# Kernel tuning notes

Hardware: AMD Instinct MI355X
Metric: run time of the kernel (lower is better)

Reference implementation:

```python
import jax, jax.numpy as jnp
import numpy as np

N_NODES = 100000
IN_DIM = 256
HIDDEN = 256
EMBED = 128
N_EDGES = 500000


def setup_inputs() -> dict:
    key = jax.random.key(0)
    ks = jax.random.split(key, 16)
    inp = {
        "h": jax.random.normal(ks[0], (N_NODES, IN_DIM), dtype=jnp.float32),
        "pos_src": jax.random.randint(ks[1], (N_EDGES,), 0, N_NODES),
        "pos_dst": jax.random.randint(ks[2], (N_EDGES,), 0, N_NODES),
        "neg_src": jax.random.randint(ks[3], (N_EDGES,), 0, N_NODES),
        "neg_dst": jax.random.randint(ks[4], (N_EDGES,), 0, N_NODES),
        "node_embeddings": jax.random.normal(ks[5], (N_NODES, EMBED), dtype=jnp.float32) * 0.1,
        # nn.Linear params (torch convention: W [out, in], y = x @ W.T + b)
        "W_pos": jax.random.normal(ks[6], (HIDDEN, IN_DIM), dtype=jnp.float32) / np.sqrt(IN_DIM),
        "b_pos": jnp.zeros((HIDDEN,), dtype=jnp.float32),
        "W_neg": jax.random.normal(ks[7], (HIDDEN, IN_DIM), dtype=jnp.float32) / np.sqrt(IN_DIM),
        "b_neg": jnp.zeros((HIDDEN,), dtype=jnp.float32),
        "W_self": jax.random.normal(ks[8], (HIDDEN, IN_DIM), dtype=jnp.float32) / np.sqrt(IN_DIM),
        "b_self": jnp.zeros((HIDDEN,), dtype=jnp.float32),
        "w_pos_beta": jax.random.normal(ks[9], (EMBED,), dtype=jnp.float32) * 0.01,
        "W_pos_u": jax.random.normal(ks[10], (EMBED, EMBED), dtype=jnp.float32) * 0.01,
        "alpha_pos": jnp.array(1.0, dtype=jnp.float32),
        "w_neg_beta": jax.random.normal(ks[11], (EMBED,), dtype=jnp.float32) * 0.01,
        "W_neg_u": jax.random.normal(ks[12], (EMBED, EMBED), dtype=jnp.float32) * 0.01,
        "alpha_neg": jnp.array(1.0, dtype=jnp.float32),
    }
    return inp


def _finsler_weight(emb, src, dst, w_beta, W_u, alpha):
    # d_Fk(j,i) = ||x_i - x_j||_2 + beta_k(x_j) * <x_i - x_j, W_u x_j>
    x_j = emb[src]                                  # [E, D]
    x_i = emb[dst]                                  # [E, D]
    diff = x_i - x_j
    euclid = jnp.sqrt(jnp.sum(diff * diff, axis=-1))
    alpha_k = jnp.clip(alpha, 0.1, 10.0)
    beta_k = jnp.tanh(x_j @ w_beta)                 # [E]
    u_j = x_j @ W_u                                 # [E, D]
    asym = jnp.sum(diff * u_j, axis=-1)             # [E]
    d = euclid + beta_k * asym
    return jnp.exp(-alpha_k * jnp.maximum(d, 0.0))  # [E]


def _agg(h, src, dst, W, b, w, n):
    # gather -> linear -> weight -> scatter-add over dst
    msg = (h[src] @ W.T + b) * w[:, None]           # [E, H]
    return jax.ops.segment_sum(msg, dst, num_segments=n)


def reference(h, pos_src, pos_dst, neg_src, neg_dst, node_embeddings,
              W_pos, b_pos, W_neg, b_neg, W_self, b_self,
              w_pos_beta, W_pos_u, alpha_pos, w_neg_beta, W_neg_u, alpha_neg):
    n = h.shape[0]
    pos_w = _finsler_weight(node_embeddings, pos_src, pos_dst, w_pos_beta, W_pos_u, alpha_pos)
    neg_w = _finsler_weight(node_embeddings, neg_src, neg_dst, w_neg_beta, W_neg_u, alpha_neg)
    pos_msg = _agg(h, pos_src, pos_dst, W_pos, b_pos, pos_w, n)
    neg_msg = _agg(h, neg_src, neg_dst, W_neg, b_neg, neg_w, n)
    self_msg = h @ W_self.T + b_self
    return jax.nn.relu(pos_msg + neg_msg + self_msg)
```

## Files before the change

### kernel.cpp

```cpp
#include <hip/hip_runtime.h>
#include <hip/hip_bf16.h>
#include <stdint.h>

#define IN_DIM 256
#define HIDDEN 256
#define EMBED 128

__global__ __launch_bounds__(256) void gemm_bt(
    const float* __restrict__ A, const float* __restrict__ W,
    const float* __restrict__ bias, float* __restrict__ C,
    int M, int N, int K)
{
    __shared__ float Ast[16][68];
    __shared__ float Wst[16][68];
    const int tid = threadIdx.x;
    const int tx = tid & 15, ty = tid >> 4;
    const int m0 = blockIdx.x * 64, n0 = blockIdx.y * 64;

    const int lm = tid >> 2;
    const int lk = (tid & 3) << 2;

    float acc[4][4] = {};

    for (int k0 = 0; k0 < K; k0 += 16) {
        float4 av = make_float4(0.f, 0.f, 0.f, 0.f);
        const int am = m0 + lm;
        if (am < M) av = *(const float4*)&A[(size_t)am * K + k0 + lk];
        const float4 wv = *(const float4*)&W[(size_t)(n0 + lm) * K + k0 + lk];
        __syncthreads();
        Ast[lk + 0][lm] = av.x; Ast[lk + 1][lm] = av.y;
        Ast[lk + 2][lm] = av.z; Ast[lk + 3][lm] = av.w;
        Wst[lk + 0][lm] = wv.x; Wst[lk + 1][lm] = wv.y;
        Wst[lk + 2][lm] = wv.z; Wst[lk + 3][lm] = wv.w;
        __syncthreads();
#pragma unroll
        for (int k = 0; k < 16; ++k) {
            const float4 a = *(const float4*)&Ast[k][ty * 4];
            const float4 b = *(const float4*)&Wst[k][tx * 4];
            acc[0][0] += a.x * b.x; acc[0][1] += a.x * b.y; acc[0][2] += a.x * b.z; acc[0][3] += a.x * b.w;
            acc[1][0] += a.y * b.x; acc[1][1] += a.y * b.y; acc[1][2] += a.y * b.z; acc[1][3] += a.y * b.w;
            acc[2][0] += a.z * b.x; acc[2][1] += a.z * b.y; acc[2][2] += a.z * b.z; acc[2][3] += a.z * b.w;
            acc[3][0] += a.w * b.x; acc[3][1] += a.w * b.y; acc[3][2] += a.w * b.z; acc[3][3] += a.w * b.w;
        }
    }

    const float4 bv = *(const float4*)&bias[n0 + tx * 4];
#pragma unroll
    for (int i = 0; i < 4; ++i) {
        const int m = m0 + ty * 4 + i;
        if (m < M) {
            float4 o;
            o.x = acc[i][0] + bv.x; o.y = acc[i][1] + bv.y;
            o.z = acc[i][2] + bv.z; o.w = acc[i][3] + bv.w;
            *(float4*)&C[(size_t)m * N + n0 + tx * 4] = o;
        }
    }
}

__global__ __launch_bounds__(256) void gemm_nn(
    const float* __restrict__ A, const float* __restrict__ B,
    float* __restrict__ C, int M, int N, int K)
{
    __shared__ float Ast[16][68];
    __shared__ float Bs[16][68];
    const int tid = threadIdx.x;
    const int tx = tid & 15, ty = tid >> 4;
    const int m0 = blockIdx.x * 64, n0 = blockIdx.y * 64;

    const int lm = tid >> 2;
    const int lk = (tid & 3) << 2;
    const int bk = tid >> 4;
    const int bn = (tid & 15) << 2;

    float acc[4][4] = {};

    for (int k0 = 0; k0 < K; k0 += 16) {
        float4 av = make_float4(0.f, 0.f, 0.f, 0.f);
        const int am = m0 + lm;
        if (am < M) av = *(const float4*)&A[(size_t)am * K + k0 + lk];
        const float4 bvl = *(const float4*)&B[(size_t)(k0 + bk) * N + n0 + bn];
        __syncthreads();
        Ast[lk + 0][lm] = av.x; Ast[lk + 1][lm] = av.y;
        Ast[lk + 2][lm] = av.z; Ast[lk + 3][lm] = av.w;
        *(float4*)&Bs[bk][bn] = bvl;
        __syncthreads();
#pragma unroll
        for (int k = 0; k < 16; ++k) {
            const float4 a = *(const float4*)&Ast[k][ty * 4];
            const float4 b = *(const float4*)&Bs[k][tx * 4];
            acc[0][0] += a.x * b.x; acc[0][1] += a.x * b.y; acc[0][2] += a.x * b.z; acc[0][3] += a.x * b.w;
            acc[1][0] += a.y * b.x; acc[1][1] += a.y * b.y; acc[1][2] += a.y * b.z; acc[1][3] += a.y * b.w;
            acc[2][0] += a.z * b.x; acc[2][1] += a.z * b.y; acc[2][2] += a.z * b.z; acc[2][3] += a.z * b.w;
            acc[3][0] += a.w * b.x; acc[3][1] += a.w * b.y; acc[3][2] += a.w * b.z; acc[3][3] += a.w * b.w;
        }
    }

#pragma unroll
    for (int i = 0; i < 4; ++i) {
        const int m = m0 + ty * 4 + i;
        if (m < M) {
            float4 o;
            o.x = acc[i][0]; o.y = acc[i][1]; o.z = acc[i][2]; o.w = acc[i][3];
            *(float4*)&C[(size_t)m * N + n0 + tx * 4] = o;
        }
    }
}

__global__ __launch_bounds__(256) void edge_weight(
    const float* __restrict__ emb, const float* __restrict__ U,
    const float* __restrict__ w_beta, const float* __restrict__ alpha_p,
    const int* __restrict__ src, const int* __restrict__ dst,
    float* __restrict__ w_out, int E)
{
    const int wv = (int)((blockIdx.x * (size_t)blockDim.x + threadIdx.x) >> 6);
    const int lane = threadIdx.x & 63;
    if (wv >= E) return;
    const int s = src[wv], d = dst[wv];

    const float* xj = emb + (size_t)s * EMBED;
    const float* xi = emb + (size_t)d * EMBED;
    const float* uj = U + (size_t)s * EMBED;

    const float xj0 = xj[lane], xj1 = xj[lane + 64];
    const float xi0 = xi[lane], xi1 = xi[lane + 64];
    const float u0 = uj[lane],  u1 = uj[lane + 64];
    const float wb0 = w_beta[lane], wb1 = w_beta[lane + 64];

    const float d0 = xi0 - xj0, d1 = xi1 - xj1;
    float pe = d0 * d0 + d1 * d1;
    float pa = d0 * u0 + d1 * u1;
    float pb = xj0 * wb0 + xj1 * wb1;

#pragma unroll
    for (int off = 32; off > 0; off >>= 1) {
        pe += __shfl_xor(pe, off);
        pa += __shfl_xor(pa, off);
        pb += __shfl_xor(pb, off);
    }

    if (lane == 0) {
        const float alpha = fminf(fmaxf(alpha_p[0], 0.1f), 10.0f);
        const float beta = tanhf(pb);
        const float dist = sqrtf(pe) + beta * pa;
        w_out[wv] = expf(-alpha * fmaxf(dist, 0.0f));
    }
}

__global__ __launch_bounds__(256) void zero_int(int* __restrict__ p, int n)
{
    const int i = blockIdx.x * blockDim.x + threadIdx.x;
    if (i < n) p[i] = 0;
}

__global__ __launch_bounds__(256) void hist(
    const int* __restrict__ dst, int* __restrict__ counts, int E)
{
    const int e = blockIdx.x * blockDim.x + threadIdx.x;
    if (e < E) atomicAdd(&counts[dst[e]], 1);
}

__global__ __launch_bounds__(256) void scan1(
    const int* __restrict__ counts, int* __restrict__ offs,
    int* __restrict__ bsum, int n)
{
    __shared__ int wsum[4];
    const int t = threadIdx.x;
    const int gi = blockIdx.x * 1024 + t * 4;
    int v[4];
#pragma unroll
    for (int j = 0; j < 4; ++j) v[j] = (gi + j < n) ? counts[gi + j] : 0;
    const int local = v[0] + v[1] + v[2] + v[3];
    const int lane = t & 63;
    int x = local;
#pragma unroll
    for (int off = 1; off < 64; off <<= 1) {
        const int y = __shfl_up(x, off);
        if (lane >= off) x += y;
    }
    if (lane == 63) wsum[t >> 6] = x;
    __syncthreads();
    int woff = 0;
    const int wid = t >> 6;
    for (int w = 0; w < wid; ++w) woff += wsum[w];
    int run = woff + x - local;
#pragma unroll
    for (int j = 0; j < 4; ++j) {
        if (gi + j < n) offs[gi + j] = run;
        run += v[j];
    }
    if (t == 255) bsum[blockIdx.x] = woff + x;
}

__global__ __launch_bounds__(128) void scan2(int* __restrict__ bsum, int nb)
{
    __shared__ int tmp[128];
    const int t = threadIdx.x;
    tmp[t] = (t < nb) ? bsum[t] : 0;
    __syncthreads();
    if (t < nb) {
        int s = 0;
        for (int i = 0; i < t; ++i) s += tmp[i];
        bsum[t] = s;
    }
}

__global__ __launch_bounds__(256) void scan3(
    int* __restrict__ offs, int* __restrict__ cur,
    const int* __restrict__ bsum, int n, int E)
{
    const int gi = blockIdx.x * blockDim.x + threadIdx.x;
    if (gi < n) {
        const int v = offs[gi] + bsum[gi >> 10];
        offs[gi] = v;
        cur[gi] = v;
    }
    if (gi == 0) offs[n] = E;
}

__global__ __launch_bounds__(256) void place(
    const int* __restrict__ src, const int* __restrict__ dst,
    const float* __restrict__ w, int* __restrict__ cur,
    int* __restrict__ esrc, float* __restrict__ ew, int E)
{
    const int e = blockIdx.x * blockDim.x + threadIdx.x;
    if (e < E) {
        const int p = atomicAdd(&cur[dst[e]], 1);
        esrc[p] = src[e];
        ew[p] = w[e];
    }
}

template <bool RELU>
__global__ __launch_bounds__(256) void gather(
    const float* __restrict__ H, const int* __restrict__ offs,
    const int* __restrict__ esrc, const float* __restrict__ ew,
    float* __restrict__ out, int n)
{
    const int node = (int)((blockIdx.x * (size_t)blockDim.x + threadIdx.x) >> 6);
    const int lane = threadIdx.x & 63;
    if (node >= n) return;
    const int s0 = offs[node], s1 = offs[node + 1];

    float4 acc = make_float4(0.f, 0.f, 0.f, 0.f);
    for (int k = s0; k < s1; ++k) {
        const int s = esrc[k];
        const float wv = ew[k];
        const float4 v = *(const float4*)&H[(size_t)s * HIDDEN + lane * 4];
        acc.x += v.x * wv; acc.y += v.y * wv;
        acc.z += v.z * wv; acc.w += v.w * wv;
    }

    float* o = out + (size_t)node * HIDDEN + lane * 4;
    float4 c = *(const float4*)o;
    c.x += acc.x; c.y += acc.y; c.z += acc.z; c.w += acc.w;
    if (RELU) {
        c.x = fmaxf(c.x, 0.f); c.y = fmaxf(c.y, 0.f);
        c.z = fmaxf(c.z, 0.f); c.w = fmaxf(c.w, 0.f);
    }
    *(float4*)o = c;
}

extern "C" void kernel_launch(void* const* d_in, const int* in_sizes, int n_in,
                              void* d_out, int out_size, void* d_ws, size_t ws_size,
                              hipStream_t stream)
{
    const float* h        = (const float*)d_in[0];
    const int*   pos_src  = (const int*)d_in[1];
    const int*   pos_dst  = (const int*)d_in[2];
    const int*   neg_src  = (const int*)d_in[3];
    const int*   neg_dst  = (const int*)d_in[4];
    const float* emb      = (const float*)d_in[5];
    const float* W_pos    = (const float*)d_in[6];
    const float* b_pos    = (const float*)d_in[7];
    const float* W_neg    = (const float*)d_in[8];
    const float* b_neg    = (const float*)d_in[9];
    const float* W_self   = (const float*)d_in[10];
    const float* b_self   = (const float*)d_in[11];
    const float* w_pos_b  = (const float*)d_in[12];
    const float* W_pos_u  = (const float*)d_in[13];
    const float* alpha_p  = (const float*)d_in[14];
    const float* w_neg_b  = (const float*)d_in[15];
    const float* W_neg_u  = (const float*)d_in[16];
    const float* alpha_n  = (const float*)d_in[17];
    float* out = (float*)d_out;

    const int n_nodes = in_sizes[0] / IN_DIM;
    const int E       = in_sizes[1];

    float* ws     = (float*)d_ws;
    float* wpos   = ws;
    float* wneg   = wpos + E;
    int*   counts = (int*)(wneg + E);
    int*   offs   = counts + n_nodes;
    int*   cur    = offs + n_nodes + 1;
    int*   bsum   = cur + n_nodes;
    int*   esrc   = bsum + 128;
    float* ew     = (float*)(esrc + E);
    float* Hbuf   = (float*)(((uintptr_t)(ew + E) + 15) & ~(uintptr_t)15);
    float* Ubuf   = Hbuf;

    const dim3 blk(256);
    const dim3 gU((n_nodes + 63) / 64, EMBED / 64);
    const dim3 gH((n_nodes + 63) / 64, HIDDEN / 64);
    const dim3 gE((E + 3) / 4);
    const dim3 gEt((E + 255) / 256);
    const dim3 gN((n_nodes + 255) / 256);
    const dim3 gW((n_nodes + 3) / 4);
    const int  nb = (n_nodes + 1023) / 1024;

    gemm_nn<<<gU, blk, 0, stream>>>(emb, W_pos_u, Ubuf, n_nodes, EMBED, EMBED);
    edge_weight<<<gE, blk, 0, stream>>>(emb, Ubuf, w_pos_b, alpha_p,
                                        pos_src, pos_dst, wpos, E);
    gemm_nn<<<gU, blk, 0, stream>>>(emb, W_neg_u, Ubuf, n_nodes, EMBED, EMBED);
    edge_weight<<<gE, blk, 0, stream>>>(emb, Ubuf, w_neg_b, alpha_n,
                                        neg_src, neg_dst, wneg, E);

    gemm_bt<<<gH, blk, 0, stream>>>(h, W_self, b_self, out, n_nodes, HIDDEN, IN_DIM);

    zero_int<<<gN, blk, 0, stream>>>(counts, n_nodes);
    hist<<<gEt, blk, 0, stream>>>(pos_dst, counts, E);
    scan1<<<nb, blk, 0, stream>>>(counts, offs, bsum, n_nodes);
    scan2<<<1, 128, 0, stream>>>(bsum, nb);
    scan3<<<gN, blk, 0, stream>>>(offs, cur, bsum, n_nodes, E);
    place<<<gEt, blk, 0, stream>>>(pos_src, pos_dst, wpos, cur, esrc, ew, E);
    gemm_bt<<<gH, blk, 0, stream>>>(h, W_pos, b_pos, Hbuf, n_nodes, HIDDEN, IN_DIM);
    gather<false><<<gW, blk, 0, stream>>>(Hbuf, offs, esrc, ew, out, n_nodes);

    zero_int<<<gN, blk, 0, stream>>>(counts, n_nodes);
    hist<<<gEt, blk, 0, stream>>>(neg_dst, counts, E);
    scan1<<<nb, blk, 0, stream>>>(counts, offs, bsum, n_nodes);
    scan2<<<1, 128, 0, stream>>>(bsum, nb);
    scan3<<<gN, blk, 0, stream>>>(offs, cur, bsum, n_nodes, E);
    place<<<gEt, blk, 0, stream>>>(neg_src, neg_dst, wneg, cur, esrc, ew, E);
    gemm_bt<<<gH, blk, 0, stream>>>(h, W_neg, b_neg, Hbuf, n_nodes, HIDDEN, IN_DIM);
    gather<true><<<gW, blk, 0, stream>>>(Hbuf, offs, esrc, ew, out, n_nodes);
}
```

Baseline: 1.479 ms.

## Aggregate raw features before projection and fuse three GEMMs into one split-bf16 MFMA kernel

Uses linearity to gather and weight raw h rows per destination first, instead of projecting every node and then gathering. All three linear layers (pos, neg, self) then run as one concatenated-K GEMM, with the bias scaled by the per-node weight sums and ReLU applied in the epilogue. The GEMM moves from scalar FP32 FMA to bf16 MFMA using a hi/lo split with three products to keep near-FP32 accuracy, and the weights are pre-split in small kernels on each call. This removes two full HIDDEN-wide intermediate buffers and the read-modify-write passes over out, but adds two aggregated-feature buffers and B operands loaded straight from global memory without LDS reuse.

```diff
diff --git a/kernel.cpp b/kernel.cpp
--- a/kernel.cpp
+++ b/kernel.cpp
@@ -6,53 +6,103 @@
 #define HIDDEN 256
 #define EMBED 128
 
-__global__ __launch_bounds__(256) void gemm_bt(
-    const float* __restrict__ A, const float* __restrict__ W,
-    const float* __restrict__ bias, float* __restrict__ C,
-    int M, int N, int K)
-{
-    __shared__ float Ast[16][68];
-    __shared__ float Wst[16][68];
-    const int tid = threadIdx.x;
-    const int tx = tid & 15, ty = tid >> 4;
-    const int m0 = blockIdx.x * 64, n0 = blockIdx.y * 64;
-
-    const int lm = tid >> 2;
-    const int lk = (tid & 3) << 2;
-
-    float acc[4][4] = {};
-
-    for (int k0 = 0; k0 < K; k0 += 16) {
-        float4 av = make_float4(0.f, 0.f, 0.f, 0.f);
-        const int am = m0 + lm;
-        if (am < M) av = *(const float4*)&A[(size_t)am * K + k0 + lk];
-        const float4 wv = *(const float4*)&W[(size_t)(n0 + lm) * K + k0 + lk];
-        __syncthreads();
-        Ast[lk + 0][lm] = av.x; Ast[lk + 1][lm] = av.y;
-        Ast[lk + 2][lm] = av.z; Ast[lk + 3][lm] = av.w;
-        Wst[lk + 0][lm] = wv.x; Wst[lk + 1][lm] = wv.y;
-        Wst[lk + 2][lm] = wv.z; Wst[lk + 3][lm] = wv.w;
-        __syncthreads();
-#pragma unroll
-        for (int k = 0; k < 16; ++k) {
-            const float4 a = *(const float4*)&Ast[k][ty * 4];
-            const float4 b = *(const float4*)&Wst[k][tx * 4];
-            acc[0][0] += a.x * b.x; acc[0][1] += a.x * b.y; acc[0][2] += a.x * b.z; acc[0][3] += a.x * b.w;
-            acc[1][0] += a.y * b.x; acc[1][1] += a.y * b.y; acc[1][2] += a.y * b.z; acc[1][3] += a.y * b.w;
-            acc[2][0] += a.z * b.x; acc[2][1] += a.z * b.y; acc[2][2] += a.z * b.z; acc[2][3] += a.z * b.w;
-            acc[3][0] += a.w * b.x; acc[3][1] += a.w * b.y; acc[3][2] += a.w * b.z; acc[3][3] += a.w * b.w;
+using bf16x8 = __attribute__((ext_vector_type(8))) short;
+using f32x4  = __attribute__((ext_vector_type(4))) float;
+
+__device__ inline void split_bf16(float x, unsigned short& hb, unsigned short& lb)
+{
+    unsigned int u = __float_as_uint(x);
+    unsigned int r = u + 0x7fffu + ((u >> 16) & 1u);
+    hb = (unsigned short)(r >> 16);
+    float fh = __uint_as_float((unsigned int)hb << 16);
+    float xl = x - fh;
+    unsigned int ul = __float_as_uint(xl);
+    unsigned int rl = ul + 0x7fffu + ((ul >> 16) & 1u);
+    lb = (unsigned short)(rl >> 16);
+}
+
+__global__ __launch_bounds__(256) void conv_w(
+    const float* __restrict__ src, unsigned short* __restrict__ hi,
+    unsigned short* __restrict__ lo, int n)
+{
+    const int i = blockIdx.x * 256 + threadIdx.x;
+    if (i < n) {
+        unsigned short hb, lb;
+        split_bf16(src[i], hb, lb);
+        hi[i] = hb; lo[i] = lb;
+    }
+}
+
+__global__ __launch_bounds__(256) void mega_gemm(
+    const float* __restrict__ aggP, const float* __restrict__ aggN,
+    const float* __restrict__ h,
+    const unsigned short* __restrict__ Whi, const unsigned short* __restrict__ Wlo,
+    const float* __restrict__ b_pos, const float* __restrict__ b_neg,
+    const float* __restrict__ b_self,
+    const float* __restrict__ sw_pos, const float* __restrict__ sw_neg,
+    float* __restrict__ out, int M)
+{
+    const int tid  = threadIdx.x;
+    const int lane = tid & 63;
+    const int wid  = tid >> 6;
+    const int lr   = lane & 15;
+    const int lg   = lane >> 4;
+    const int m0   = blockIdx.x * 64;
+
+    const int rowA = min(m0 + wid * 16 + lr, M - 1);
+    const float* As[3] = {aggP, aggN, h};
+
+    f32x4 acc[16];
+#pragma unroll
+    for (int i = 0; i < 16; ++i) acc[i] = (f32x4){0.f, 0.f, 0.f, 0.f};
+
+#pragma unroll
+    for (int seg = 0; seg < 3; ++seg) {
+        const float* A = As[seg] + (size_t)rowA * 256;
+        const unsigned short* WH = Whi + seg * 65536;
+        const unsigned short* WL = Wlo + seg * 65536;
+        for (int ks = 0; ks < 8; ++ks) {
+            const int kc = ks * 32 + lg * 8;
+            const float4 x0 = *(const float4*)(A + kc);
+            const float4 x1 = *(const float4*)(A + kc + 4);
+            const float xs[8] = {x0.x, x0.y, x0.z, x0.w, x1.x, x1.y, x1.z, x1.w};
+            bf16x8 ah, al;
+#pragma unroll
+            for (int j = 0; j < 8; ++j) {
+                unsigned short hb, lb;
+                split_bf16(xs[j], hb, lb);
+                ah[j] = (short)hb;
+                al[j] = (short)lb;
+            }
+#pragma unroll
+            for (int nf = 0; nf < 16; ++nf) {
+                const size_t wo = (size_t)(nf * 16 + lr) * 256 + kc;
+                const bf16x8 bh = *(const bf16x8*)(WH + wo);
+                const bf16x8 bl = *(const bf16x8*)(WL + wo);
+                acc[nf] = __builtin_amdgcn_mfma_f32_16x16x32_bf16(ah, bh, acc[nf], 0, 0, 0);
+                acc[nf] = __builtin_amdgcn_mfma_f32_16x16x32_bf16(ah, bl, acc[nf], 0, 0, 0);
+                acc[nf] = __builtin_amdgcn_mfma_f32_16x16x32_bf16(al, bh, acc[nf], 0, 0, 0);
+            }
         }
     }
 
-    const float4 bv = *(const float4*)&bias[n0 + tx * 4];
+    float bp[16], bn[16], bs[16];
+#pragma unroll
+    for (int nf = 0; nf < 16; ++nf) {
+        const int col = nf * 16 + lr;
+        bp[nf] = b_pos[col]; bn[nf] = b_neg[col]; bs[nf] = b_self[col];
+    }
 #pragma unroll
     for (int i = 0; i < 4; ++i) {
-        const int m = m0 + ty * 4 + i;
-        if (m < M) {
-            float4 o;
-            o.x = acc[i][0] + bv.x; o.y = acc[i][1] + bv.y;
-            o.z = acc[i][2] + bv.z; o.w = acc[i][3] + bv.w;
-            *(float4*)&C[(size_t)m * N + n0 + tx * 4] = o;
+        const int r = m0 + wid * 16 + lg * 4 + i;
+        if (r < M) {
+            const float swp = sw_pos[r], swn = sw_neg[r];
+#pragma unroll
+            for (int nf = 0; nf < 16; ++nf) {
+                const int col = nf * 16 + lr;
+                const float v = acc[nf][i] + swp * bp[nf] + swn * bn[nf] + bs[nf];
+                out[(size_t)r * 256 + col] = fmaxf(v, 0.f);
+            }
         }
     }
 }
@@ -230,11 +280,10 @@
     }
 }
 
-template <bool RELU>
-__global__ __launch_bounds__(256) void gather(
-    const float* __restrict__ H, const int* __restrict__ offs,
+__global__ __launch_bounds__(256) void gather_h(
+    const float* __restrict__ h, const int* __restrict__ offs,
     const int* __restrict__ esrc, const float* __restrict__ ew,
-    float* __restrict__ out, int n)
+    float* __restrict__ agg, float* __restrict__ sw, int n)
 {
     const int node = (int)((blockIdx.x * (size_t)blockDim.x + threadIdx.x) >> 6);
     const int lane = threadIdx.x & 63;
@@ -242,22 +291,18 @@
     const int s0 = offs[node], s1 = offs[node + 1];
 
     float4 acc = make_float4(0.f, 0.f, 0.f, 0.f);
+    float s = 0.f;
     for (int k = s0; k < s1; ++k) {
-        const int s = esrc[k];
+        const int sr = esrc[k];
         const float wv = ew[k];
-        const float4 v = *(const float4*)&H[(size_t)s * HIDDEN + lane * 4];
+        const float4 v = *(const float4*)&h[(size_t)sr * IN_DIM + lane * 4];
         acc.x += v.x * wv; acc.y += v.y * wv;
         acc.z += v.z * wv; acc.w += v.w * wv;
-    }
-
-    float* o = out + (size_t)node * HIDDEN + lane * 4;
-    float4 c = *(const float4*)o;
-    c.x += acc.x; c.y += acc.y; c.z += acc.z; c.w += acc.w;
-    if (RELU) {
-        c.x = fmaxf(c.x, 0.f); c.y = fmaxf(c.y, 0.f);
-        c.z = fmaxf(c.z, 0.f); c.w = fmaxf(c.w, 0.f);
-    }
-    *(float4*)o = c;
+        s += wv;
+    }
+
+    *(float4*)&agg[(size_t)node * IN_DIM + lane * 4] = acc;
+    if (lane == 0) sw[node] = s;
 }
 
 extern "C" void kernel_launch(void* const* d_in, const int* in_sizes, int n_in,
@@ -287,26 +332,35 @@
     const int n_nodes = in_sizes[0] / IN_DIM;
     const int E       = in_sizes[1];
 
-    float* ws     = (float*)d_ws;
-    float* wpos   = ws;
-    float* wneg   = wpos + E;
-    int*   counts = (int*)(wneg + E);
+    float* ws    = (float*)d_ws;
+    float* aggP  = ws;
+    float* aggN  = aggP + (size_t)n_nodes * 256;
+    float* wpos  = aggN + (size_t)n_nodes * 256;
+    float* wneg  = wpos + E;
+    float* swp   = wneg + E;
+    float* swn   = swp + n_nodes;
+    int*   counts = (int*)(swn + n_nodes);
     int*   offs   = counts + n_nodes;
-    int*   cur    = offs + n_nodes + 1;
+    int*   cur    = offs + n_nodes + 4;
     int*   bsum   = cur + n_nodes;
     int*   esrc   = bsum + 128;
     float* ew     = (float*)(esrc + E);
-    float* Hbuf   = (float*)(((uintptr_t)(ew + E) + 15) & ~(uintptr_t)15);
-    float* Ubuf   = Hbuf;
+    unsigned short* Whi = (unsigned short*)(ew + E);
+    unsigned short* Wlo = Whi + 3 * 65536;
+    float* Ubuf  = aggP;
 
     const dim3 blk(256);
     const dim3 gU((n_nodes + 63) / 64, EMBED / 64);
-    const dim3 gH((n_nodes + 63) / 64, HIDDEN / 64);
     const dim3 gE((E + 3) / 4);
     const dim3 gEt((E + 255) / 256);
     const dim3 gN((n_nodes + 255) / 256);
     const dim3 gW((n_nodes + 3) / 4);
+    const dim3 gG((n_nodes + 63) / 64);
     const int  nb = (n_nodes + 1023) / 1024;
+
+    conv_w<<<256, blk, 0, stream>>>(W_pos,  Whi,             Wlo,             65536);
+    conv_w<<<256, blk, 0, stream>>>(W_neg,  Whi + 65536,     Wlo + 65536,     65536);
+    conv_w<<<256, blk, 0, stream>>>(W_self, Whi + 2 * 65536, Wlo + 2 * 65536, 65536);
 
     gemm_nn<<<gU, blk, 0, stream>>>(emb, W_pos_u, Ubuf, n_nodes, EMBED, EMBED);
     edge_weight<<<gE, blk, 0, stream>>>(emb, Ubuf, w_pos_b, alpha_p,
@@ -315,16 +369,13 @@
     edge_weight<<<gE, blk, 0, stream>>>(emb, Ubuf, w_neg_b, alpha_n,
                                         neg_src, neg_dst, wneg, E);
 
-    gemm_bt<<<gH, blk, 0, stream>>>(h, W_self, b_self, out, n_nodes, HIDDEN, IN_DIM);
-
     zero_int<<<gN, blk, 0, stream>>>(counts, n_nodes);
     hist<<<gEt, blk, 0, stream>>>(pos_dst, counts, E);
     scan1<<<nb, blk, 0, stream>>>(counts, offs, bsum, n_nodes);
     scan2<<<1, 128, 0, stream>>>(bsum, nb);
     scan3<<<gN, blk, 0, stream>>>(offs, cur, bsum, n_nodes, E);
     place<<<gEt, blk, 0, stream>>>(pos_src, pos_dst, wpos, cur, esrc, ew, E);
-    gemm_bt<<<gH, blk, 0, stream>>>(h, W_pos, b_pos, Hbuf, n_nodes, HIDDEN, IN_DIM);
-    gather<false><<<gW, blk, 0, stream>>>(Hbuf, offs, esrc, ew, out, n_nodes);
+    gather_h<<<gW, blk, 0, stream>>>(h, offs, esrc, ew, aggP, swp, n_nodes);
 
     zero_int<<<gN, blk, 0, stream>>>(counts, n_nodes);
     hist<<<gEt, blk, 0, stream>>>(neg_dst, counts, E);
@@ -332,6 +383,9 @@
     scan2<<<1, 128, 0, stream>>>(bsum, nb);
     scan3<<<gN, blk, 0, stream>>>(offs, cur, bsum, n_nodes, E);
     place<<<gEt, blk, 0, stream>>>(neg_src, neg_dst, wneg, cur, esrc, ew, E);
-    gemm_bt<<<gH, blk, 0, stream>>>(h, W_neg, b_neg, Hbuf, n_nodes, HIDDEN, IN_DIM);
-    gather<true><<<gW, blk, 0, stream>>>(Hbuf, offs, esrc, ew, out, n_nodes);
-}
+    gather_h<<<gW, blk, 0, stream>>>(h, offs, esrc, ew, aggN, swn, n_nodes);
+
+    mega_gemm<<<gG, blk, 0, stream>>>(aggP, aggN, h, Whi, Wlo,
+                                      b_pos, b_neg, b_self, swp, swn,
+                                      out, n_nodes);
+}
```

Measured after the change: 1.587 ms. 1.07x slower.
